# Optimization experiments

Measured on AMD Instinct MI355X. Metric: run time of the kernel, lower is better.

Reference implementation:

```python
import jax, jax.numpy as jnp
import numpy as np

T, B, H, L = 256, 64, 1024, 2
P = 0.1  # dropout prob


def setup_inputs() -> dict:
    key = jax.random.key(0)
    ks = jax.random.split(key, 7)
    s = 1.0 / np.sqrt(H)  # matches uniform(-1/sqrt(H), 1/sqrt(H)) scale
    x = jax.random.normal(ks[0], (T, B, H), dtype=jnp.float32)
    W_ih = jax.random.uniform(ks[1], (L, 4 * H, H), jnp.float32, -s, s)
    W_hh = jax.random.uniform(ks[2], (L, 4 * H, H), jnp.float32, -s, s)
    b_ih = jax.random.uniform(ks[3], (L, 4 * H), jnp.float32, -s, s)
    b_hh = jax.random.uniform(ks[4], (L, 4 * H), jnp.float32, -s, s)
    keep = 1.0 - P
    # torch code samples a fresh bernoulli mask each call (per timestep)
    mask_h = jax.random.bernoulli(ks[5], keep, (L, T, B, H)).astype(jnp.float32) / keep
    mask_in = jax.random.bernoulli(ks[6], keep, (L - 1, T, B, H)).astype(jnp.float32) / keep
    return {"x": x, "W_ih": W_ih, "W_hh": W_hh, "b_ih": b_ih, "b_hh": b_hh,
            "mask_h": mask_h, "mask_in": mask_in}


def _lstm_layer(x_seq, Wih, Whh, bih, bhh, mh_seq):
    # x_seq: [T,B,I], Wih: [4H,I], Whh: [4H,H], mh_seq: [T,B,H]
    t, b = x_seq.shape[0], x_seq.shape[1]
    h = Whh.shape[1]
    # precompute input contribution for all timesteps: [T,B,4H]
    pre = jnp.einsum('tbi,gi->tbg', x_seq, Wih) + bih + bhh

    def step(carry, inputs):
        h_prev, c_prev = carry
        pre_t, mh_t = inputs
        gates = pre_t + (h_prev * mh_t) @ Whh.T  # [B,4H]
        i, f, g, o = jnp.split(gates, 4, axis=-1)
        c = jax.nn.sigmoid(f) * c_prev + jax.nn.sigmoid(i) * jnp.tanh(g)
        hn = jax.nn.sigmoid(o) * jnp.tanh(c)
        return (hn, c), (hn, c)

    init = (jnp.zeros((b, h), x_seq.dtype), jnp.zeros((b, h), x_seq.dtype))
    _, (h_seq, c_seq) = jax.lax.scan(step, init, (pre, mh_seq))
    return h_seq, c_seq  # each [T,B,H]


def reference(x, W_ih, W_hh, b_ih, b_hh, mask_h, mask_in):
    n_layers = W_ih.shape[0]
    inp = x
    c_seq = None
    for l in range(n_layers):
        if l > 0:
            inp = inp * mask_in[l - 1]  # inter-layer variational dropout
        inp, c_seq = _lstm_layer(inp, W_ih[l], W_hh[l], b_ih[l], b_hh[l], mask_h[l])
    # torch module returns (output, (h_n[-1], c_n[-1])); h_n[-1] == output
    return inp, inp, c_seq
```

## Files before the change

kernel.cpp:

```cpp
#include <hip/hip_runtime.h>


#define T_STEPS 256
#define BATCH   64
#define HID     1024
#define G4      4096
#define OUTSZ   (T_STEPS * BATCH * HID)

typedef _Float16 half8 __attribute__((ext_vector_type(8)));
typedef _Float16 half4 __attribute__((ext_vector_type(4)));
typedef float    f32x4 __attribute__((ext_vector_type(4)));

__device__ __forceinline__ float sigm(float x) { return 1.0f / (1.0f + __expf(-x)); }

__global__ __launch_bounds__(256) void zero_ws(float* p, int n) {
    int i = blockIdx.x * 256 + threadIdx.x;
    if (i < n) p[i] = 0.0f;
}

__global__ __launch_bounds__(256) void split_w(
    const float* __restrict__ wih, const float* __restrict__ whh,
    _Float16* __restrict__ wih_hi, _Float16* __restrict__ wih_lo,
    _Float16* __restrict__ whh_hi, _Float16* __restrict__ whh_lo)
{
    int i = blockIdx.x * 256 + threadIdx.x;
    {
        float4 a = ((const float4*)wih)[i];
        half4 h, l;
        h[0] = (_Float16)a.x; l[0] = (_Float16)(a.x - (float)h[0]);
        h[1] = (_Float16)a.y; l[1] = (_Float16)(a.y - (float)h[1]);
        h[2] = (_Float16)a.z; l[2] = (_Float16)(a.z - (float)h[2]);
        h[3] = (_Float16)a.w; l[3] = (_Float16)(a.w - (float)h[3]);
        ((half4*)wih_hi)[i] = h; ((half4*)wih_lo)[i] = l;
    }
    {
        float4 a = ((const float4*)whh)[i];
        half4 h, l;
        h[0] = (_Float16)a.x; l[0] = (_Float16)(a.x - (float)h[0]);
        h[1] = (_Float16)a.y; l[1] = (_Float16)(a.y - (float)h[1]);
        h[2] = (_Float16)a.z; l[2] = (_Float16)(a.z - (float)h[2]);
        h[3] = (_Float16)a.w; l[3] = (_Float16)(a.w - (float)h[3]);
        ((half4*)whh_hi)[i] = h; ((half4*)whh_lo)[i] = l;
    }
}

__global__ __launch_bounds__(256) void pre_gemm(
    const float* __restrict__ A, const float* __restrict__ Amask, int row0,
    const _Float16* __restrict__ Bhi, const _Float16* __restrict__ Blo,
    const float* __restrict__ bih, const float* __restrict__ bhh,
    float* __restrict__ preOut)
{
    __shared__ _Float16 As [128][40];
    __shared__ _Float16 BsH[128][40];
    __shared__ _Float16 BsL[128][40];

    const int bm = blockIdx.x, bn = blockIdx.y;
    const int tid = threadIdx.x;
    const int wave = tid >> 6, lane = tid & 63;
    const int wm = wave & 1, wn = wave >> 1;
    const int lr = lane & 15, kq = lane >> 4;

    f32x4 acc[4][4] = {};

    const int mrow = tid >> 3;
    const int k4   = (tid & 7) * 4;
    const int nrow = tid >> 1;
    const int kb   = (tid & 1) * 16;

    for (int kk = 0; kk < 32; ++kk) {
        const int k0 = kk * 32;
        #pragma unroll
        for (int mi = 0; mi < 4; ++mi) {
            const int m = mrow + mi * 32;
            const size_t gofs = (size_t)(row0 + bm * 128 + m) * 1024 + k0 + k4;
            float4 av = *(const float4*)(A + gofs);
            if (Amask) {
                float4 mv = *(const float4*)(Amask + gofs);
                av.x *= mv.x; av.y *= mv.y; av.z *= mv.z; av.w *= mv.w;
            }
            half4 hv;
            hv[0] = (_Float16)av.x; hv[1] = (_Float16)av.y;
            hv[2] = (_Float16)av.z; hv[3] = (_Float16)av.w;
            *(half4*)&As[m][k4] = hv;
        }
        {
            const size_t gofs = (size_t)(bn * 128 + nrow) * 1024 + k0 + kb;
            half8 b0 = *(const half8*)(Bhi + gofs);
            half8 b1 = *(const half8*)(Bhi + gofs + 8);
            *(half8*)&BsH[nrow][kb]     = b0;
            *(half8*)&BsH[nrow][kb + 8] = b1;
            half8 c0 = *(const half8*)(Blo + gofs);
            half8 c1 = *(const half8*)(Blo + gofs + 8);
            *(half8*)&BsL[nrow][kb]     = c0;
            *(half8*)&BsL[nrow][kb + 8] = c1;
        }
        __syncthreads();

        half8 af[4], bh[4], bl[4];
        #pragma unroll
        for (int i = 0; i < 4; ++i)
            af[i] = *(const half8*)&As[wm * 64 + i * 16 + lr][kq * 8];
        #pragma unroll
        for (int j = 0; j < 4; ++j) {
            bh[j] = *(const half8*)&BsH[wn * 64 + j * 16 + lr][kq * 8];
            bl[j] = *(const half8*)&BsL[wn * 64 + j * 16 + lr][kq * 8];
        }
        #pragma unroll
        for (int i = 0; i < 4; ++i)
            #pragma unroll
            for (int j = 0; j < 4; ++j) {
                acc[i][j] = __builtin_amdgcn_mfma_f32_16x16x32_f16(af[i], bl[j], acc[i][j], 0, 0, 0);
                acc[i][j] = __builtin_amdgcn_mfma_f32_16x16x32_f16(af[i], bh[j], acc[i][j], 0, 0, 0);
            }
        __syncthreads();
    }

    #pragma unroll
    for (int j = 0; j < 4; ++j) {
        const int g = bn * 128 + wn * 64 + j * 16 + lr;
        const float bias = bih[g] + bhh[g];
        #pragma unroll
        for (int i = 0; i < 4; ++i) {
            const int rb = bm * 128 + wm * 64 + i * 16 + kq * 4;
            #pragma unroll
            for (int r = 0; r < 4; ++r)
                preOut[(size_t)(rb + r) * G4 + g] = acc[i][j][r] + bias;
        }
    }
}

__global__ __launch_bounds__(256) void scan_step(
    const float*    __restrict__ preT,
    const _Float16* __restrict__ WhhHi,
    const _Float16* __restrict__ WhhLo,
    const _Float16* __restrict__ hmIn,
    _Float16*       __restrict__ hmOut,
    const float*    __restrict__ maskNext,
    float*          __restrict__ cbuf,
    float*          __restrict__ hOutA,
    float*          __restrict__ hOutB,
    float*          __restrict__ cOut)
{
    __shared__ float gl[16][68];

    const int wg = blockIdx.x;
    const int j0 = wg * 4;
    const int tid = threadIdx.x;
    const int wave = tid >> 6, lane = tid & 63;
    const int lr = lane & 15, kq = lane >> 4;

    const int grow = (lr >> 2) * HID + j0 + (lr & 3);
    const int bcol = wave * 16 + lr;

    f32x4 acc = {0.f, 0.f, 0.f, 0.f};
    const _Float16* wh = WhhHi + (size_t)grow * HID;
    const _Float16* wl = WhhLo + (size_t)grow * HID;
    const _Float16* hv = hmIn + (size_t)bcol * HID;

    #pragma unroll 4
    for (int kk = 0; kk < 32; ++kk) {
        const int k0 = kk * 32 + kq * 8;
        half8 ah = *(const half8*)(wh + k0);
        half8 al = *(const half8*)(wl + k0);
        half8 bb = *(const half8*)(hv + k0);
        acc = __builtin_amdgcn_mfma_f32_16x16x32_f16(al, bb, acc, 0, 0, 0);
        acc = __builtin_amdgcn_mfma_f32_16x16x32_f16(ah, bb, acc, 0, 0, 0);
    }

    #pragma unroll
    for (int r = 0; r < 4; ++r)
        gl[kq * 4 + r][wave * 16 + lr] = acc[r];
    __syncthreads();

    const int jj = tid & 3;
    const int b  = tid >> 2;
    const int j  = j0 + jj;

    const float gi = gl[jj     ][b] + preT[(size_t)b * G4 + j];
    const float gf = gl[4  + jj][b] + preT[(size_t)b * G4 + HID + j];
    const float gg = gl[8  + jj][b] + preT[(size_t)b * G4 + 2 * HID + j];
    const float go = gl[12 + jj][b] + preT[(size_t)b * G4 + 3 * HID + j];

    const float si = sigm(gi);
    const float sf = sigm(gf);
    const float sg = tanhf(gg);
    const float so = sigm(go);

    const size_t bj = (size_t)b * HID + j;
    const float cprev = cbuf[bj];
    const float c = sf * cprev + si * sg;
    const float h = so * tanhf(c);
    cbuf[bj] = c;

    hOutA[bj] = h;
    if (hOutB) hOutB[bj] = h;
    if (cOut)  cOut[bj]  = c;
    if (maskNext) hmOut[bj] = (_Float16)(h * maskNext[bj]);
}

extern "C" void kernel_launch(void* const* d_in, const int* in_sizes, int n_in,
                              void* d_out, int out_size, void* d_ws, size_t ws_size,
                              hipStream_t stream)
{
    const float* x       = (const float*)d_in[0];
    const float* W_ih    = (const float*)d_in[1];
    const float* W_hh    = (const float*)d_in[2];
    const float* b_ih    = (const float*)d_in[3];
    const float* b_hh    = (const float*)d_in[4];
    const float* mask_h  = (const float*)d_in[5];
    const float* mask_in = (const float*)d_in[6];

    float* out0 = (float*)d_out;
    float* out1 = out0 + (size_t)OUTSZ;
    float* out2 = out0 + 2 * (size_t)OUTSZ;

    char* ws = (char*)d_ws;
    size_t off = 0;
    auto alloc = [&](size_t bytes) { void* p = ws + off; off += (bytes + 255) & ~(size_t)255; return p; };

    const size_t WELEM = (size_t)2 * G4 * HID;
    _Float16* wih_hi = (_Float16*)alloc(WELEM * 2);
    _Float16* wih_lo = (_Float16*)alloc(WELEM * 2);
    _Float16* whh_hi = (_Float16*)alloc(WELEM * 2);
    _Float16* whh_lo = (_Float16*)alloc(WELEM * 2);
    float*    pre    = (float*)alloc((size_t)64 * BATCH * G4 * 4);
    _Float16* hm     = (_Float16*)alloc((size_t)2 * BATCH * HID * 2);
    float*    cbuf   = (float*)alloc((size_t)BATCH * HID * 4);
    (void)ws_size; (void)in_sizes; (void)n_in; (void)out_size;

    split_w<<<8192, 256, 0, stream>>>(W_ih, W_hh, wih_hi, wih_lo, whh_hi, whh_lo);

    for (int l = 0; l < 2; ++l) {
        zero_ws<<<512, 256, 0, stream>>>((float*)hm, 131072);

        const float* Ain = l ? out1 : x;
        const float* Am  = l ? mask_in : nullptr;
        const _Float16* BH = wih_hi + (size_t)l * G4 * HID;
        const _Float16* BL = wih_lo + (size_t)l * G4 * HID;
        const _Float16* WH = whh_hi + (size_t)l * G4 * HID;
        const _Float16* WL = whh_lo + (size_t)l * G4 * HID;
        const float* bi = b_ih + l * G4;
        const float* bh = b_hh + l * G4;

        for (int c = 0; c < 4; ++c) {
            pre_gemm<<<dim3(32, 32), 256, 0, stream>>>(Ain, Am, c * 4096, BH, BL, bi, bh, pre);
            for (int tt = 0; tt < 64; ++tt) {
                const int t = c * 64 + tt;
                const float* mnext = (t < T_STEPS - 1)
                    ? mask_h + ((size_t)(l * T_STEPS + t + 1) * BATCH) * HID : nullptr;
                float* hA = (l ? out0 : out1) + (size_t)t * BATCH * HID;
                float* hB = l ? out1 + (size_t)t * BATCH * HID : nullptr;
                float* cO = l ? out2 + (size_t)t * BATCH * HID : nullptr;
                scan_step<<<256, 256, 0, stream>>>(
                    pre + (size_t)tt * BATCH * G4,
                    WH, WL,
                    hm + (size_t)(t & 1) * BATCH * HID,
                    hm + (size_t)((t + 1) & 1) * BATCH * HID,
                    mnext, cbuf, hA, hB, cO);
            }
        }
    }
}
```

Measured before the change: 10.15 ms.

## Fuse per-timestep scan launches into a persistent chunk kernel with grid barrier

Replaces 64 separate scan_step launches per chunk with one persistent scan_chunk kernel that loops over 64 timesteps and synchronises all 256 workgroups through a two-level atomic grid barrier. Each block keeps its slice of the recurrent weights (hi/lo fp16 splits) in registers across timesteps and carries the cell state in a register instead of reloading it from global memory. The pre-gate GEMM output is re-laid out per gate so the fused kernel can read the four gates with simple strides. This removes launch overhead and repeated weight loads, but relies on all 256 blocks being co-resident, uses heavy register pressure (launch_bounds 256,1), and adds spin-wait barrier latency each step.

```diff
diff --git a/kernel.cpp b/kernel.cpp
--- a/kernel.cpp
+++ b/kernel.cpp
@@ -6,6 +6,7 @@
 #define HID     1024
 #define G4      4096
 #define OUTSZ   (T_STEPS * BATCH * HID)
+#define BH_     65536
 
 typedef _Float16 half8 __attribute__((ext_vector_type(8)));
 typedef _Float16 half4 __attribute__((ext_vector_type(4)));
@@ -116,86 +117,128 @@
     }
 
     #pragma unroll
-    for (int j = 0; j < 4; ++j) {
-        const int g = bn * 128 + wn * 64 + j * 16 + lr;
+    for (int j4 = 0; j4 < 4; ++j4) {
+        const int g = bn * 128 + wn * 64 + j4 * 16 + lr;
+        const int gate = g >> 10, jc = g & 1023;
         const float bias = bih[g] + bhh[g];
         #pragma unroll
         for (int i = 0; i < 4; ++i) {
-            const int rb = bm * 128 + wm * 64 + i * 16 + kq * 4;
+            const int rbase = bm * 128 + wm * 64 + i * 16 + kq * 4;
             #pragma unroll
-            for (int r = 0; r < 4; ++r)
-                preOut[(size_t)(rb + r) * G4 + g] = acc[i][j][r] + bias;
-        }
-    }
-}
-
-__global__ __launch_bounds__(256) void scan_step(
-    const float*    __restrict__ preT,
+            for (int r = 0; r < 4; ++r) {
+                const int rloc = rbase + r;
+                preOut[((size_t)(rloc >> 6) * 4 + gate) * BH_ + ((rloc & 63) << 10) + jc]
+                    = acc[i][j4][r] + bias;
+            }
+        }
+    }
+}
+
+__global__ __launch_bounds__(256, 1) void scan_chunk(
+    const float*    __restrict__ pre2,
     const _Float16* __restrict__ WhhHi,
     const _Float16* __restrict__ WhhLo,
-    const _Float16* __restrict__ hmIn,
-    _Float16*       __restrict__ hmOut,
-    const float*    __restrict__ maskNext,
+    _Float16*       __restrict__ hm,
+    const float*    __restrict__ maskL,
     float*          __restrict__ cbuf,
-    float*          __restrict__ hOutA,
-    float*          __restrict__ hOutB,
-    float*          __restrict__ cOut)
+    float*          __restrict__ hA,
+    float*          __restrict__ hB,
+    float*          __restrict__ cO,
+    int tBase, int phaseBase,
+    unsigned int*   __restrict__ bar)
 {
-    __shared__ float gl[16][68];
-
-    const int wg = blockIdx.x;
-    const int j0 = wg * 4;
-    const int tid = threadIdx.x;
-    const int wave = tid >> 6, lane = tid & 63;
-    const int lr = lane & 15, kq = lane >> 4;
-
-    const int grow = (lr >> 2) * HID + j0 + (lr & 3);
-    const int bcol = wave * 16 + lr;
-
-    f32x4 acc = {0.f, 0.f, 0.f, 0.f};
-    const _Float16* wh = WhhHi + (size_t)grow * HID;
-    const _Float16* wl = WhhLo + (size_t)grow * HID;
-    const _Float16* hv = hmIn + (size_t)bcol * HID;
-
-    #pragma unroll 4
-    for (int kk = 0; kk < 32; ++kk) {
-        const int k0 = kk * 32 + kq * 8;
-        half8 ah = *(const half8*)(wh + k0);
-        half8 al = *(const half8*)(wl + k0);
-        half8 bb = *(const half8*)(hv + k0);
-        acc = __builtin_amdgcn_mfma_f32_16x16x32_f16(al, bb, acc, 0, 0, 0);
-        acc = __builtin_amdgcn_mfma_f32_16x16x32_f16(ah, bb, acc, 0, 0, 0);
-    }
-
-    #pragma unroll
-    for (int r = 0; r < 4; ++r)
-        gl[kq * 4 + r][wave * 16 + lr] = acc[r];
-    __syncthreads();
-
-    const int jj = tid & 3;
-    const int b  = tid >> 2;
-    const int j  = j0 + jj;
-
-    const float gi = gl[jj     ][b] + preT[(size_t)b * G4 + j];
-    const float gf = gl[4  + jj][b] + preT[(size_t)b * G4 + HID + j];
-    const float gg = gl[8  + jj][b] + preT[(size_t)b * G4 + 2 * HID + j];
-    const float go = gl[12 + jj][b] + preT[(size_t)b * G4 + 3 * HID + j];
-
-    const float si = sigm(gi);
-    const float sf = sigm(gf);
-    const float sg = tanhf(gg);
-    const float so = sigm(go);
-
+    const int wg   = blockIdx.x;
+    const int j0   = wg << 2;
+    const int tid  = threadIdx.x;
+    const int w    = tid >> 6;
+    const int lane = tid & 63;
+    const int lr   = lane & 15;
+    const int kq   = lane >> 4;
+
+    const int grow = (lr & 3) * HID + j0 + (lr >> 2);
+
+    half8 wh[32], wl[32];
+    {
+        const _Float16* whp = WhhHi + (size_t)grow * HID + kq * 8;
+        const _Float16* wlp = WhhLo + (size_t)grow * HID + kq * 8;
+        #pragma unroll
+        for (int kk = 0; kk < 32; ++kk) {
+            wh[kk] = *(const half8*)(whp + kk * 32);
+            wl[kk] = *(const half8*)(wlp + kk * 32);
+        }
+    }
+
+    const int b  = (w << 4) + lr;
+    const int j  = j0 + kq;
     const size_t bj = (size_t)b * HID + j;
-    const float cprev = cbuf[bj];
-    const float c = sf * cprev + si * sg;
-    const float h = so * tanhf(c);
-    cbuf[bj] = c;
-
-    hOutA[bj] = h;
-    if (hOutB) hOutB[bj] = h;
-    if (cOut)  cOut[bj]  = c;
-    if (maskNext) hmOut[bj] = (_Float16)(h * maskNext[bj]);
+
+    float creg = cbuf[bj];
+
+    for (int tt = 0; tt < 64; ++tt) {
+        const int t = tBase + tt;
+
+        if (tt > 0) {
+            __builtin_amdgcn_fence(__ATOMIC_RELEASE, "agent");
+            __syncthreads();
+            if (tid == 0) {
+                const unsigned int phase = (unsigned int)(phaseBase + tt - 1);
+                unsigned int old = atomicAdd(&bar[(wg & 7) * 32], 1u);
+                if (old == 32u * (phase + 1u) - 1u)
+                    atomicAdd(&bar[256], 1u);
+                while (__hip_atomic_load(&bar[256], __ATOMIC_RELAXED,
+                                         __HIP_MEMORY_SCOPE_AGENT) < 8u * (phase + 1u))
+                    __builtin_amdgcn_s_sleep(2);
+            }
+            __syncthreads();
+            __builtin_amdgcn_fence(__ATOMIC_ACQUIRE, "agent");
+        }
+
+        const _Float16* bp = hm + (size_t)(t & 1) * BH_ + ((size_t)b << 10) + kq * 8;
+
+        f32x4 aL[4] = {{0.f,0.f,0.f,0.f},{0.f,0.f,0.f,0.f},{0.f,0.f,0.f,0.f},{0.f,0.f,0.f,0.f}};
+        f32x4 aH[4] = {{0.f,0.f,0.f,0.f},{0.f,0.f,0.f,0.f},{0.f,0.f,0.f,0.f},{0.f,0.f,0.f,0.f}};
+        half8 bb[16];
+        #pragma unroll
+        for (int kk = 0; kk < 16; ++kk) bb[kk] = *(const half8*)(bp + kk * 32);
+        #pragma unroll
+        for (int kk = 0; kk < 16; ++kk) {
+            aL[kk & 3] = __builtin_amdgcn_mfma_f32_16x16x32_f16(wl[kk], bb[kk], aL[kk & 3], 0, 0, 0);
+            aH[kk & 3] = __builtin_amdgcn_mfma_f32_16x16x32_f16(wh[kk], bb[kk], aH[kk & 3], 0, 0, 0);
+        }
+        #pragma unroll
+        for (int kk = 0; kk < 16; ++kk) bb[kk] = *(const half8*)(bp + 512 + kk * 32);
+        #pragma unroll
+        for (int kk = 0; kk < 16; ++kk) {
+            aL[kk & 3] = __builtin_amdgcn_mfma_f32_16x16x32_f16(wl[kk + 16], bb[kk], aL[kk & 3], 0, 0, 0);
+            aH[kk & 3] = __builtin_amdgcn_mfma_f32_16x16x32_f16(wh[kk + 16], bb[kk], aH[kk & 3], 0, 0, 0);
+        }
+
+        f32x4 g4 = ((aL[0] + aL[1]) + (aL[2] + aL[3])) + ((aH[0] + aH[1]) + (aH[2] + aH[3]));
+
+        const float* pt = pre2 + (size_t)tt * (4 * BH_) + ((size_t)b << 10) + j;
+        const float gi = g4[0] + pt[0];
+        const float gf = g4[1] + pt[BH_];
+        const float gg = g4[2] + pt[2 * BH_];
+        const float go = g4[3] + pt[3 * BH_];
+
+        const float si = sigm(gi);
+        const float sf = sigm(gf);
+        const float tg = tanhf(gg);
+        const float so = sigm(go);
+
+        creg = sf * creg + si * tg;
+        const float h = so * tanhf(creg);
+
+        const size_t tbj = (size_t)t * BH_ + bj;
+        hA[tbj] = h;
+        if (hB) hB[tbj] = h;
+        if (cO) cO[tbj] = creg;
+        if (t < T_STEPS - 1) {
+            _Float16* hnxt = hm + (size_t)((t + 1) & 1) * BH_;
+            hnxt[bj] = (_Float16)(h * maskL[(size_t)(t + 1) * BH_ + bj]);
+        }
+    }
+    cbuf[bj] = creg;
 }
 
 extern "C" void kernel_launch(void* const* d_in, const int* in_sizes, int n_in,
@@ -224,11 +267,13 @@
     _Float16* whh_hi = (_Float16*)alloc(WELEM * 2);
     _Float16* whh_lo = (_Float16*)alloc(WELEM * 2);
     float*    pre    = (float*)alloc((size_t)64 * BATCH * G4 * 4);
-    _Float16* hm     = (_Float16*)alloc((size_t)2 * BATCH * HID * 2);
-    float*    cbuf   = (float*)alloc((size_t)BATCH * HID * 4);
+    _Float16* hm     = (_Float16*)alloc((size_t)2 * BH_ * 2);
+    float*    cbuf   = (float*)alloc((size_t)BH_ * 4);
+    unsigned int* bar = (unsigned int*)alloc(4096);
     (void)ws_size; (void)in_sizes; (void)n_in; (void)out_size;
 
     split_w<<<8192, 256, 0, stream>>>(W_ih, W_hh, wih_hi, wih_lo, whh_hi, whh_lo);
+    zero_ws<<<2, 256, 0, stream>>>((float*)bar, 512);
 
     for (int l = 0; l < 2; ++l) {
         zero_ws<<<512, 256, 0, stream>>>((float*)hm, 131072);
@@ -241,23 +286,17 @@
         const _Float16* WL = whh_lo + (size_t)l * G4 * HID;
         const float* bi = b_ih + l * G4;
         const float* bh = b_hh + l * G4;
+        const float* maskL = mask_h + (size_t)l * OUTSZ;
+
+        float* hA = l ? out0 : out1;
+        float* hB = l ? out1 : nullptr;
+        float* cO = l ? out2 : nullptr;
 
         for (int c = 0; c < 4; ++c) {
             pre_gemm<<<dim3(32, 32), 256, 0, stream>>>(Ain, Am, c * 4096, BH, BL, bi, bh, pre);
-            for (int tt = 0; tt < 64; ++tt) {
-                const int t = c * 64 + tt;
-                const float* mnext = (t < T_STEPS - 1)
-                    ? mask_h + ((size_t)(l * T_STEPS + t + 1) * BATCH) * HID : nullptr;
-                float* hA = (l ? out0 : out1) + (size_t)t * BATCH * HID;
-                float* hB = l ? out1 + (size_t)t * BATCH * HID : nullptr;
-                float* cO = l ? out2 + (size_t)t * BATCH * HID : nullptr;
-                scan_step<<<256, 256, 0, stream>>>(
-                    pre + (size_t)tt * BATCH * G4,
-                    WH, WL,
-                    hm + (size_t)(t & 1) * BATCH * HID,
-                    hm + (size_t)((t + 1) & 1) * BATCH * HID,
-                    mnext, cbuf, hA, hB, cO);
-            }
-        }
-    }
-}
+            scan_chunk<<<256, 256, 0, stream>>>(pre, WH, WL, hm, maskL, cbuf,
+                                                hA, hB, cO,
+                                                c * 64, (l * 4 + c) * 63, bar);
+        }
+    }
+}
```

New measurement: 21.17 ms. 2.09x slower.
